# Optimization experiments

Hardware: AMD Instinct MI355X
Metric: run time of the kernel (lower is better)

## Reference

```python
import jax, jax.numpy as jnp
import numpy as np

NUM_CODES = 128
BETA = 0.25


def conv1d(x, w, b):
    # x: (B, C, T), w: (O, I, K) torch layout, 'same' padding for k=3
    y = jax.lax.conv_general_dilated(x, w, window_strides=(1,), padding=[(1, 1)],
                                     dimension_numbers=('NCH', 'OIH', 'NCH'))
    return y + b[None, :, None]


def setup_inputs() -> dict:
    key = jax.random.key(0)
    ks = jax.random.split(key, 8)
    B, C, T, K = 16, 192, 8192, NUM_CODES
    fan = 1.0 / np.sqrt(C * 3)
    inp = {
        'x': jax.random.normal(ks[0], (B, C, T), jnp.float32),
        'enc_w1': jax.random.normal(ks[1], (C, C, 3), jnp.float32) * fan,
        'enc_b1': jnp.zeros((C,), jnp.float32),
        'enc_w2': jax.random.normal(ks[2], (C, C, 3), jnp.float32) * fan,
        'enc_b2': jnp.zeros((C,), jnp.float32),
        'emb': jax.random.normal(ks[3], (K, C), jnp.float32) * (1.0 / K),
        'dec_w1': jax.random.normal(ks[4], (C, C, 3), jnp.float32) * fan,
        'dec_b1': jnp.zeros((C,), jnp.float32),
        'dec_w2': jax.random.normal(ks[5], (C, C, 3), jnp.float32) * fan,
        'dec_b2': jnp.zeros((C,), jnp.float32),
        'dec_w3': jax.random.normal(ks[6], (C, C, 3), jnp.float32) * fan,
        'dec_b3': jnp.zeros((C,), jnp.float32),
    }
    return inp


def vector_quantize(z_e, emb):
    # z_e: (B, C, T) -> tokens (B*T, C)
    B, C, T = z_e.shape
    z = jnp.transpose(z_e, (0, 2, 1)).reshape(-1, C)          # (N, C)
    # squared distances ||z||^2 + ||e||^2 - 2 z.e
    d = (jnp.sum(z * z, axis=1, keepdims=True)
         + jnp.sum(emb * emb, axis=1)[None, :]
         - 2.0 * (z @ emb.T))                                  # (N, K)
    idx = jnp.argmin(d, axis=1)                                # (N,)
    z_q = emb[idx]                                             # (N, C) gather
    # loss = ||sg(z_q) - z||^2*... standard: codebook + beta*commitment
    loss = (jnp.mean((jax.lax.stop_gradient(z_q) - z) ** 2)
            + BETA * jnp.mean((z_q - jax.lax.stop_gradient(z)) ** 2))
    # perplexity of code usage
    n = z.shape[0]
    counts = jnp.zeros((emb.shape[0],), z.dtype).at[idx].add(1.0)
    probs = counts / n
    perplexity = jnp.exp(-jnp.sum(probs * jnp.log(probs + 1e-10)))
    # straight-through
    z_q = z + jax.lax.stop_gradient(z_q - z)
    z_q = jnp.transpose(z_q.reshape(B, T, C), (0, 2, 1))
    return loss, z_q, perplexity, idx


def reference(x, enc_w1, enc_b1, enc_w2, enc_b2, emb,
              dec_w1, dec_b1, dec_w2, dec_b2, dec_w3, dec_b3):
    # encoder: conv -> relu -> conv
    z_e = conv1d(jax.nn.relu(conv1d(x, enc_w1, enc_b1)), enc_w2, enc_b2)
    embedding_loss, z_q, perplexity, _ = vector_quantize(z_e, emb)
    # NOTE: source forward decodes z_e (not z_q) — reproduced faithfully
    h = jax.nn.relu(conv1d(z_e, dec_w1, dec_b1))
    h = jax.nn.relu(conv1d(h, dec_w2, dec_b2))
    x_hat = conv1d(h, dec_w3, dec_b3)
    return embedding_loss, x_hat, perplexity
```

## Files before the change

### kernel.cpp

```cpp
#include <hip/hip_runtime.h>
#include <hip/hip_bf16.h>
#include <stdint.h>

typedef short s16x8 __attribute__((ext_vector_type(8)));
typedef float f32x4 __attribute__((ext_vector_type(4)));
typedef unsigned int u32;
typedef unsigned short u16;

#define CCH 192
#define APITCH 200
#define NCODES 128
#define HALO 9
#define RPB 8216
#define LEAD 12
#define TOK 128
#define AROWS 146
#define WSTRIDE 40960

__device__ __forceinline__ u16 f2b(float f) {
  u32 u = __builtin_bit_cast(u32, f);
  u = (u + 0x7fffu + ((u >> 16) & 1u)) >> 16;
  return (u16)u;
}
__device__ __forceinline__ float b2f(u16 h) {
  return __builtin_bit_cast(float, ((u32)h) << 16);
}
__device__ __forceinline__ void gld16(const void* g, void* l) {
  __builtin_amdgcn_global_load_lds(
      (const __attribute__((address_space(1))) void*)g,
      (__attribute__((address_space(3))) void*)l, 16, 0, 0);
}

__global__ __launch_bounds__(256) void k_tin(const float* __restrict__ x, u16* __restrict__ xtp,
                                             int B, int T) {
  __shared__ float tile[32][36];
  int nt = T >> 5;
  int bid = blockIdx.x;
  int b = bid / (6 * nt);
  int rem = bid % (6 * nt);
  int cb = rem / nt, tb = rem % nt;
  int tid = threadIdx.x;
  {
    int c = tid >> 3, seg = tid & 7;
    const float* src = x + ((size_t)b * CCH + cb * 32 + c) * T + tb * 32 + seg * 4;
    float4 v = *(const float4*)src;
    tile[c][seg * 4 + 0] = v.x; tile[c][seg * 4 + 1] = v.y;
    tile[c][seg * 4 + 2] = v.z; tile[c][seg * 4 + 3] = v.w;
  }
  __syncthreads();
  {
    int t = tid >> 3, cs = tid & 7;
    u16* dst = xtp + ((size_t)(b * RPB + LEAD + tb * 32 + t)) * APITCH + cb * 32 + cs * 4;
    ushort4 o;
    o.x = f2b(tile[cs * 4 + 0][t]); o.y = f2b(tile[cs * 4 + 1][t]);
    o.z = f2b(tile[cs * 4 + 2][t]); o.w = f2b(tile[cs * 4 + 3][t]);
    *(ushort4*)dst = o;
  }
}

__global__ __launch_bounds__(256) void k_padz(u16* __restrict__ xtp) {
  int b = blockIdx.x;
  for (int i = threadIdx.x; i < 24 * 25; i += 256) {
    int r = i / 25, c = i - (i / 25) * 25;
    int row = (r < 12) ? r : (RPB - 12 + (r - 12));
    uint4 z = {0u, 0u, 0u, 0u};
    *(uint4*)((char*)xtp + ((size_t)(b * RPB + row)) * 400 + c * 16) = z;
  }
}

__global__ __launch_bounds__(256) void k_wconv(const float* __restrict__ w, u16* __restrict__ dst) {
  int i = blockIdx.x * 256 + threadIdx.x;
  if (i >= 3 * CCH * CCH) return;
  int cb = i / 18432;
  int r = i - cb * 18432;
  int k = r / 6144;
  int r2 = r - k * 6144;
  int o = r2 / 32, il = r2 - o * 32;
  dst[cb * 20480 + k * 6144 + (il >> 3) * 1536 + o * 8 + (il & 7)] =
      f2b(w[(o * CCH + cb * 32 + il) * 3 + k]);
}

__global__ __launch_bounds__(64) void k_emb(const float* __restrict__ emb, u16* __restrict__ embp,
                                            float* __restrict__ e2) {
  int code = blockIdx.x, lane = threadIdx.x;
  float s = 0.f;
  for (int j = lane * 3; j < lane * 3 + 3; ++j) {
    float v = emb[code * CCH + j];
    embp[code * APITCH + j] = f2b(v);
    s += v * v;
  }
  if (lane < 8) embp[code * APITCH + 192 + lane] = 0;
  #pragma unroll
  for (int m = 1; m < 64; m <<= 1) s += __shfl_xor(s, m, 64);
  if (lane == 0) e2[code] = s;
}

__global__ void k_zero(int* hist, double* dsum) {
  int t = threadIdx.x;
  if (t < NCODES) hist[t] = 0;
  if (t == 0) *dsum = 0.0;
}

template<int G0, bool RELU, bool ISSUE_NEXT>
__device__ __forceinline__ void stage(const char* __restrict__ wtp, u16* __restrict__ act,
                                      u16 (*wb)[20480], const float* bv,
                                      int oB, const u16* arow, int rbase,
                                      int wv, int lane, int lr, int lg,
                                      int t0, int T, bool edge) {
  f32x4 acc[5][3];
  #pragma unroll
  for (int m = 0; m < 5; ++m)
    #pragma unroll
    for (int n = 0; n < 3; ++n) acc[m][n] = f32x4{0.f, 0.f, 0.f, 0.f};
  #pragma unroll
  for (int cb = 0; cb < 6; ++cb) {
    const int g = G0 + cb;
    asm volatile("s_waitcnt vmcnt(0)" ::: "memory");
    __builtin_amdgcn_sched_barrier(0);
    __builtin_amdgcn_s_barrier();
    if (cb < 5 || ISSUE_NEXT) {
      const char* src = wtp + (size_t)(g + 1) * WSTRIDE + (wv * 5) * 1024 + lane * 16;
      char* dst = (char*)wb[(g + 1) & 1] + (wv * 5) * 1024;
      #pragma unroll
      for (int j = 0; j < 5; ++j) gld16(src + j * 1024, dst + j * 1024);
    }
    const u16* wq = wb[g & 1] + lg * 1536;
    #pragma unroll
    for (int k = 0; k < 3; ++k) {
      s16x8 af[5];
      #pragma unroll
      for (int m = 0; m < 5; ++m)
        af[m] = *(const s16x8*)(arow + (16 * m + k) * APITCH + cb * 32);
      #pragma unroll
      for (int nf = 0; nf < 3; ++nf) {
        s16x8 wf = *(const s16x8*)(wq + k * 6144 + (oB + nf * 16 + lr) * 8);
        #pragma unroll
        for (int m = 0; m < 5; ++m)
          acc[m][nf] = __builtin_amdgcn_mfma_f32_16x16x32_bf16(af[m], wf, acc[m][nf], 0, 0, 0);
      }
    }
  }
  __builtin_amdgcn_s_barrier();
  if (!edge) {
    #pragma unroll
    for (int m = 0; m < 5; ++m)
      #pragma unroll
      for (int nf = 0; nf < 3; ++nf) {
        int o = oB + nf * 16 + lr;
        #pragma unroll
        for (int r = 0; r < 4; ++r) {
          int row = rbase + 16 * m + lg * 4 + r;
          float v = acc[m][nf][r] + bv[nf];
          if (RELU) v = fmaxf(v, 0.f);
          act[row * APITCH + o] = f2b(v);
        }
      }
  } else {
    #pragma unroll
    for (int m = 0; m < 5; ++m)
      #pragma unroll
      for (int nf = 0; nf < 3; ++nf) {
        int o = oB + nf * 16 + lr;
        #pragma unroll
        for (int r = 0; r < 4; ++r) {
          int row = rbase + 16 * m + lg * 4 + r;
          int tok = t0 - HALO + row;
          float v = acc[m][nf][r] + bv[nf];
          if (RELU) v = fmaxf(v, 0.f);
          if (tok < 0 || tok >= T) v = 0.f;
          act[row * APITCH + o] = f2b(v);
        }
      }
  }
  asm volatile("s_waitcnt lgkmcnt(0)" ::: "memory");
  __builtin_amdgcn_s_barrier();
}

__global__ __launch_bounds__(512, 1) void k_fused(
    const char* __restrict__ xtp, const char* __restrict__ wtp,
    const float* __restrict__ eb1, const float* __restrict__ eb2,
    const float* __restrict__ db1, const float* __restrict__ db2, const float* __restrict__ db3,
    const char* __restrict__ embp, const float* __restrict__ e2,
    int* __restrict__ hist, double* __restrict__ dsum,
    float* __restrict__ xhat, int T) {
  __shared__ __align__(16) u16 act[AROWS * APITCH];
  __shared__ __align__(16) u16 wb[2][20480];
  __shared__ int hs[NCODES];
  __shared__ float wsum[8];
  const int tid = threadIdx.x;
  const int wv = tid >> 6, lane = tid & 63, lr = lane & 15, lg = lane >> 4;
  const int nw = wv & 3, mw = wv >> 2;
  const int bid = blockIdx.x;
  const int b = bid >> 6, tile = bid & 63;
  const int t0 = tile * TOK;
  const bool edge = (tile == 0) || (tile == 63);
  const int oB = nw * 48;
  const int rbase = 1 + mw * 64;
  const u16* arow = act + (rbase - 1 + lr) * APITCH + lg * 8;
  if (tid < NCODES) hs[tid] = 0;

  float bvv[5][3];
  #pragma unroll
  for (int nf = 0; nf < 3; ++nf) {
    int o = oB + nf * 16 + lr;
    bvv[0][nf] = eb1[o]; bvv[1][nf] = eb2[o];
    bvv[2][nf] = db1[o]; bvv[3][nf] = db2[o]; bvv[4][nf] = db3[o];
  }

  {
    const char* src = xtp + (size_t)(b * RPB + LEAD + t0 - HALO) * 400;
    #pragma unroll
    for (int s = 0; s < 8; ++s) {
      int c = tid + s * 512;
      if (c < AROWS * 25)
        gld16(src + (size_t)c * 16, (char*)act + (size_t)c * 16);
    }
  }
  {
    const char* s0 = wtp + (size_t)(wv * 5) * 1024 + lane * 16;
    char* d0 = (char*)wb[0] + (wv * 5) * 1024;
    #pragma unroll
    for (int j = 0; j < 5; ++j) gld16(s0 + j * 1024, d0 + j * 1024);
  }

  stage<0,  true,  true >(wtp, act, wb, bvv[0], oB, arow, rbase, wv, lane, lr, lg, t0, T, edge);
  stage<6,  false, false>(wtp, act, wb, bvv[1], oB, arow, rbase, wv, lane, lr, lg, t0, T, edge);

  {
    #pragma unroll
    for (int j = 0; j < 4; ++j) {
      int c = wv + 8 * j;
      if (c < 25) {
        gld16(embp + c * 1024 + lane * 16, (char*)wb[0] + c * 1024);
        gld16(embp + 25600 + c * 1024 + lane * 16, (char*)wb[1] + c * 1024);
      }
    }
    asm volatile("s_waitcnt vmcnt(0)" ::: "memory");
    __builtin_amdgcn_sched_barrier(0);
    __builtin_amdgcn_s_barrier();

    const int row = HALO + wv * 16 + lr;
    f32x4 va[8];
    #pragma unroll
    for (int n = 0; n < 8; ++n) va[n] = f32x4{0.f, 0.f, 0.f, 0.f};
    #pragma unroll
    for (int cb = 0; cb < 6; ++cb) {
      s16x8 az = *(const s16x8*)(act + row * APITCH + cb * 32 + lg * 8);
      #pragma unroll
      for (int n = 0; n < 4; ++n) {
        s16x8 e1f = *(const s16x8*)(wb[0] + (n * 16 + lr) * APITCH + cb * 32 + lg * 8);
        va[n] = __builtin_amdgcn_mfma_f32_16x16x32_bf16(az, e1f, va[n], 0, 0, 0);
        s16x8 e2f = *(const s16x8*)(wb[1] + (n * 16 + lr) * APITCH + cb * 32 + lg * 8);
        va[n + 4] = __builtin_amdgcn_mfma_f32_16x16x32_bf16(az, e2f, va[n + 4], 0, 0, 0);
      }
    }
    float z2 = 0.f;
    const u16* zr = act + row * APITCH + lg * 48;
    #pragma unroll
    for (int j = 0; j < 48; j += 8) {
      s16x8 vv = *(const s16x8*)(zr + j);
      #pragma unroll
      for (int e = 0; e < 8; ++e) { float f = b2f((u16)vv[e]); z2 += f * f; }
    }
    z2 += __shfl_xor(z2, 16, 64);
    z2 += __shfl_xor(z2, 32, 64);
    float smin[4]; int imin[4];
    #pragma unroll
    for (int r = 0; r < 4; ++r) { smin[r] = 3.4e38f; imin[r] = 0; }
    #pragma unroll
    for (int n = 0; n < 8; ++n) {
      int code = n * 16 + lr;
      float ev = e2[code];
      #pragma unroll
      for (int r = 0; r < 4; ++r) {
        float sc = ev - 2.f * va[n][r];
        if (sc < smin[r]) { smin[r] = sc; imin[r] = code; }
      }
    }
    #pragma unroll
    for (int m = 1; m < 16; m <<= 1) {
      #pragma unroll
      for (int r = 0; r < 4; ++r) {
        float so = __shfl_xor(smin[r], m, 64);
        int io = __shfl_xor(imin[r], m, 64);
        if (so < smin[r] || (so == smin[r] && io < imin[r])) { smin[r] = so; imin[r] = io; }
      }
    }
    float z2t[4];
    #pragma unroll
    for (int r = 0; r < 4; ++r) z2t[r] = __shfl(z2, lg * 4 + r, 64);
    float dpart = 0.f;
    if (lr == 0) {
      #pragma unroll
      for (int r = 0; r < 4; ++r) {
        dpart += z2t[r] + smin[r];
        atomicAdd(&hs[imin[r]], 1);
      }
    }
    #pragma unroll
    for (int m = 1; m < 64; m <<= 1) dpart += __shfl_xor(dpart, m, 64);
    if (lane == 0) wsum[wv] = dpart;
    asm volatile("s_waitcnt lgkmcnt(0)" ::: "memory");
    __builtin_amdgcn_s_barrier();
    {
      const char* s = wtp + (size_t)12 * WSTRIDE + (wv * 5) * 1024 + lane * 16;
      char* d = (char*)wb[0] + (wv * 5) * 1024;
      #pragma unroll
      for (int j = 0; j < 5; ++j) gld16(s + j * 1024, d + j * 1024);
    }
    if (tid == 0) {
      double tot = 0.0;
      #pragma unroll
      for (int w = 0; w < 8; ++w) tot += (double)wsum[w];
      atomicAdd(dsum, tot);
    }
    if (tid < NCODES && hs[tid] > 0) atomicAdd(&hist[tid], hs[tid]);
  }

  stage<12, true, true>(wtp, act, wb, bvv[2], oB, arow, rbase, wv, lane, lr, lg, t0, T, edge);
  stage<18, true, true>(wtp, act, wb, bvv[3], oB, arow, rbase, wv, lane, lr, lg, t0, T, edge);

  f32x4 acc5[4][3];
  #pragma unroll
  for (int m = 0; m < 4; ++m)
    #pragma unroll
    for (int n = 0; n < 3; ++n) acc5[m][n] = f32x4{0.f, 0.f, 0.f, 0.f};
  {
    const u16* arow3 = act + (8 + mw * 64 + lr) * APITCH + lg * 8;
    #pragma unroll
    for (int cb = 0; cb < 6; ++cb) {
      const int g = 24 + cb;
      asm volatile("s_waitcnt vmcnt(0)" ::: "memory");
      __builtin_amdgcn_sched_barrier(0);
      __builtin_amdgcn_s_barrier();
      if (cb < 5) {
        const char* src = wtp + (size_t)(g + 1) * WSTRIDE + (wv * 5) * 1024 + lane * 16;
        char* dst = (char*)wb[(g + 1) & 1] + (wv * 5) * 1024;
        #pragma unroll
        for (int j = 0; j < 5; ++j) gld16(src + j * 1024, dst + j * 1024);
      }
      const u16* wq = wb[g & 1] + lg * 1536;
      #pragma unroll
      for (int k = 0; k < 3; ++k) {
        s16x8 af[4];
        #pragma unroll
        for (int m = 0; m < 4; ++m)
          af[m] = *(const s16x8*)(arow3 + (16 * m + k) * APITCH + cb * 32);
        #pragma unroll
        for (int nf = 0; nf < 3; ++nf) {
          s16x8 wf = *(const s16x8*)(wq + k * 6144 + (oB + nf * 16 + lr) * 8);
          #pragma unroll
          for (int m = 0; m < 4; ++m)
            acc5[m][nf] = __builtin_amdgcn_mfma_f32_16x16x32_bf16(af[m], wf, acc5[m][nf], 0, 0, 0);
        }
      }
    }
  }

  float* ft = (float*)act;
  float* dstb = xhat + (size_t)b * CCH * T + t0;
  #pragma unroll
  for (int p = 0; p < 2; ++p) {
    __builtin_amdgcn_s_barrier();
    if ((nw >> 1) == p) {
      #pragma unroll
      for (int m = 0; m < 4; ++m)
        #pragma unroll
        for (int nf = 0; nf < 3; ++nf) {
          int o = (nw & 1) * 48 + nf * 16 + lr;
          #pragma unroll
          for (int r = 0; r < 4; ++r) {
            int tl = mw * 64 + 16 * m + lg * 4 + r;
            ft[o * 130 + tl] = acc5[m][nf][r] + bvv[4][nf];
          }
        }
    }
    asm volatile("s_waitcnt lgkmcnt(0)" ::: "memory");
    __builtin_amdgcn_s_barrier();
    #pragma unroll
    for (int i = 0; i < 24; ++i) {
      int s = tid + i * 512;
      int o = s >> 7, tl = s & 127;
      dstb[(size_t)(o + p * 96) * T + tl] = ft[o * 130 + tl];
    }
  }
}

__global__ __launch_bounds__(128) void k_fin(const int* __restrict__ hist,
                                             const double* __restrict__ dsum,
                                             float* __restrict__ out, int N, int ppos) {
  __shared__ float H[NCODES];
  int t = threadIdx.x;
  float p = (float)hist[t] / (float)N;
  H[t] = p * logf(p + 1e-10f);
  __syncthreads();
  if (t == 0) {
    float s = 0.f;
    for (int i = 0; i < NCODES; ++i) s += H[i];
    out[ppos] = expf(-s);
    out[0] = (float)(1.25 * (*dsum) / ((double)N * (double)CCH));
  }
}

extern "C" void kernel_launch(void* const* d_in, const int* in_sizes, int n_in,
                              void* d_out, int out_size, void* d_ws, size_t ws_size,
                              hipStream_t stream) {
  const int B = 16, T = 8192, N = B * T;
  const float* x   = (const float*)d_in[0];
  const float* ew1 = (const float*)d_in[1];
  const float* eb1 = (const float*)d_in[2];
  const float* ew2 = (const float*)d_in[3];
  const float* eb2 = (const float*)d_in[4];
  const float* emb = (const float*)d_in[5];
  const float* dw1 = (const float*)d_in[6];
  const float* db1 = (const float*)d_in[7];
  const float* dw2 = (const float*)d_in[8];
  const float* db2 = (const float*)d_in[9];
  const float* dw3 = (const float*)d_in[10];
  const float* db3 = (const float*)d_in[11];

  char* ws = (char*)d_ws;
  char*  xtp  = ws;
  char*  wtp  = ws + 52582400;
  char*  embp = ws + 53811200;
  float* e2   = (float*)(ws + 53876736);
  int*   hist = (int*)(ws + 53877248);
  double* dsum = (double*)(ws + 53877760);

  const int wblocks = (3 * CCH * CCH + 255) / 256;
  k_wconv<<<wblocks, 256, 0, stream>>>(ew1, (u16*)wtp);
  k_wconv<<<wblocks, 256, 0, stream>>>(ew2, (u16*)wtp + 6 * 20480);
  k_wconv<<<wblocks, 256, 0, stream>>>(dw1, (u16*)wtp + 12 * 20480);
  k_wconv<<<wblocks, 256, 0, stream>>>(dw2, (u16*)wtp + 18 * 20480);
  k_wconv<<<wblocks, 256, 0, stream>>>(dw3, (u16*)wtp + 24 * 20480);
  k_emb<<<NCODES, 64, 0, stream>>>(emb, (u16*)embp, e2);
  k_zero<<<1, 256, 0, stream>>>(hist, dsum);
  k_padz<<<B, 256, 0, stream>>>((u16*)xtp);
  k_tin<<<B * 6 * (T / 32), 256, 0, stream>>>(x, (u16*)xtp, B, T);

  k_fused<<<B * (T / TOK), 512, 0, stream>>>(xtp, wtp, eb1, eb2, db1, db2, db3,
                                             embp, e2, hist, dsum, (float*)d_out + 1, T);
  k_fin<<<1, 128, 0, stream>>>(hist, dsum, (float*)d_out, N, out_size - 1);
}
```

Before: 280.3 us.

## Double token tile to 256 and stream conv weights in per-tap chunks

```diff
diff --git a/kernel.cpp b/kernel.cpp
--- a/kernel.cpp
+++ b/kernel.cpp
@@ -13,9 +13,9 @@
 #define HALO 9
 #define RPB 8216
 #define LEAD 12
-#define TOK 128
-#define AROWS 146
-#define WSTRIDE 40960
+#define TOK 256
+#define AROWS 274
+#define CHS 16384
 
 __device__ __forceinline__ u16 f2b(float f) {
   u32 u = __builtin_bit_cast(u32, f);
@@ -76,7 +76,7 @@
   int k = r / 6144;
   int r2 = r - k * 6144;
   int o = r2 / 32, il = r2 - o * 32;
-  dst[cb * 20480 + k * 6144 + (il >> 3) * 1536 + o * 8 + (il & 7)] =
+  dst[(size_t)(cb * 3 + k) * (CHS / 2) + (il >> 3) * 1536 + o * 8 + (il & 7)] =
       f2b(w[(o * CCH + cb * 32 + il) * 3 + k]);
 }
 
@@ -86,10 +86,10 @@
   float s = 0.f;
   for (int j = lane * 3; j < lane * 3 + 3; ++j) {
     float v = emb[code * CCH + j];
-    embp[code * APITCH + j] = f2b(v);
+    int cb = j >> 5, il = j & 31;
+    embp[(size_t)cb * 4096 + (il >> 3) * 1024 + code * 8 + (il & 7)] = f2b(v);
     s += v * v;
   }
-  if (lane < 8) embp[code * APITCH + 192 + lane] = 0;
   #pragma unroll
   for (int m = 1; m < 64; m <<= 1) s += __shfl_xor(s, m, 64);
   if (lane == 0) e2[code] = s;
@@ -101,49 +101,54 @@
   if (t == 0) *dsum = 0.0;
 }
 
-template<int G0, bool RELU, bool ISSUE_NEXT>
-__device__ __forceinline__ void stage(const char* __restrict__ wtp, u16* __restrict__ act,
-                                      u16 (*wb)[20480], const float* bv,
-                                      int oB, const u16* arow, int rbase,
-                                      int wv, int lane, int lr, int lg,
-                                      int t0, int T, bool edge) {
-  f32x4 acc[5][3];
-  #pragma unroll
-  for (int m = 0; m < 5; ++m)
-    #pragma unroll
-    for (int n = 0; n < 3; ++n) acc[m][n] = f32x4{0.f, 0.f, 0.f, 0.f};
-  #pragma unroll
-  for (int cb = 0; cb < 6; ++cb) {
-    const int g = G0 + cb;
+__device__ __forceinline__ void issueW(const char* src, u16* dstb, int wv, int lane) {
+  const char* s0 = src + wv * 2048 + lane * 16;
+  char* d0 = (char*)dstb + wv * 2048 + lane * 16;
+  gld16(s0, d0);
+  gld16(s0 + 1024, d0 + 1024);
+}
+__device__ __forceinline__ void issueE(const char* src, u16* dstb, int tid) {
+  gld16(src + tid * 16, (char*)dstb + tid * 16);
+}
+
+template<int G0, int F, int NEXT>
+__device__ __forceinline__ void conv_phase(const char* __restrict__ wtp, const char* __restrict__ embp,
+                                           const u16* __restrict__ arow, u16 (*wb)[8192],
+                                           int oB, int lr, int lg, int wv, int lane, int tid,
+                                           f32x4 (&acc)[F][3]) {
+  #pragma unroll 2
+  for (int s = 0; s < 18; ++s) {
     asm volatile("s_waitcnt vmcnt(0)" ::: "memory");
     __builtin_amdgcn_sched_barrier(0);
     __builtin_amdgcn_s_barrier();
-    if (cb < 5 || ISSUE_NEXT) {
-      const char* src = wtp + (size_t)(g + 1) * WSTRIDE + (wv * 5) * 1024 + lane * 16;
-      char* dst = (char*)wb[(g + 1) & 1] + (wv * 5) * 1024;
-      #pragma unroll
-      for (int j = 0; j < 5; ++j) gld16(src + j * 1024, dst + j * 1024);
-    }
-    const u16* wq = wb[g & 1] + lg * 1536;
-    #pragma unroll
-    for (int k = 0; k < 3; ++k) {
-      s16x8 af[5];
-      #pragma unroll
-      for (int m = 0; m < 5; ++m)
-        af[m] = *(const s16x8*)(arow + (16 * m + k) * APITCH + cb * 32);
-      #pragma unroll
-      for (int nf = 0; nf < 3; ++nf) {
-        s16x8 wf = *(const s16x8*)(wq + k * 6144 + (oB + nf * 16 + lr) * 8);
-        #pragma unroll
-        for (int m = 0; m < 5; ++m)
-          acc[m][nf] = __builtin_amdgcn_mfma_f32_16x16x32_bf16(af[m], wf, acc[m][nf], 0, 0, 0);
-      }
-    }
-  }
+    if (s < 17) issueW(wtp + (size_t)(G0 + s + 1) * CHS, wb[(s + 1) & 1], wv, lane);
+    else if (NEXT == 1) issueW(wtp + (size_t)(G0 + 18) * CHS, wb[0], wv, lane);
+    else if (NEXT == 2) issueE(embp, wb[0], tid);
+    const int cb = s / 3, k = s - 3 * (s / 3);
+    const u16* wq = wb[s & 1] + lg * 1536 + (oB + lr) * 8;
+    const u16* ab = arow + k * APITCH + cb * 32;
+    s16x8 af[F];
+    #pragma unroll
+    for (int m = 0; m < F; ++m)
+      af[m] = *(const s16x8*)(ab + 16 * m * APITCH);
+    #pragma unroll
+    for (int nf = 0; nf < 3; ++nf) {
+      s16x8 wf = *(const s16x8*)(wq + nf * 128);
+      #pragma unroll
+      for (int m = 0; m < F; ++m)
+        acc[m][nf] = __builtin_amdgcn_mfma_f32_16x16x32_bf16(af[m], wf, acc[m][nf], 0, 0, 0);
+    }
+  }
+}
+
+template<int F, bool RELU>
+__device__ __forceinline__ void writeback(u16* __restrict__ act, const f32x4 (&acc)[F][3],
+                                          const float* bv, int oB, int lr, int lg, int rbase,
+                                          int t0, int T, bool edge) {
   __builtin_amdgcn_s_barrier();
   if (!edge) {
     #pragma unroll
-    for (int m = 0; m < 5; ++m)
+    for (int m = 0; m < F; ++m)
       #pragma unroll
       for (int nf = 0; nf < 3; ++nf) {
         int o = oB + nf * 16 + lr;
@@ -157,7 +162,7 @@
       }
   } else {
     #pragma unroll
-    for (int m = 0; m < 5; ++m)
+    for (int m = 0; m < F; ++m)
       #pragma unroll
       for (int nf = 0; nf < 3; ++nf) {
         int o = oB + nf * 16 + lr;
@@ -176,7 +181,7 @@
   __builtin_amdgcn_s_barrier();
 }
 
-__global__ __launch_bounds__(512, 1) void k_fused(
+__global__ __launch_bounds__(512, 2) void k_fused(
     const char* __restrict__ xtp, const char* __restrict__ wtp,
     const float* __restrict__ eb1, const float* __restrict__ eb2,
     const float* __restrict__ db1, const float* __restrict__ db2, const float* __restrict__ db3,
@@ -184,18 +189,18 @@
     int* __restrict__ hist, double* __restrict__ dsum,
     float* __restrict__ xhat, int T) {
   __shared__ __align__(16) u16 act[AROWS * APITCH];
-  __shared__ __align__(16) u16 wb[2][20480];
+  __shared__ __align__(16) u16 wb[2][8192];
   __shared__ int hs[NCODES];
   __shared__ float wsum[8];
   const int tid = threadIdx.x;
   const int wv = tid >> 6, lane = tid & 63, lr = lane & 15, lg = lane >> 4;
   const int nw = wv & 3, mw = wv >> 2;
   const int bid = blockIdx.x;
-  const int b = bid >> 6, tile = bid & 63;
+  const int b = bid >> 5, tile = bid & 31;
   const int t0 = tile * TOK;
-  const bool edge = (tile == 0) || (tile == 63);
+  const bool edge = (tile == 0) || (tile == 31);
   const int oB = nw * 48;
-  const int rbase = 1 + mw * 64;
+  const int rbase = 1 + mw * 128;
   const u16* arow = act + (rbase - 1 + lr) * APITCH + lg * 8;
   if (tid < NCODES) hs[tid] = 0;
 
@@ -210,91 +215,99 @@
   {
     const char* src = xtp + (size_t)(b * RPB + LEAD + t0 - HALO) * 400;
     #pragma unroll
-    for (int s = 0; s < 8; ++s) {
+    for (int s = 0; s < 14; ++s) {
       int c = tid + s * 512;
       if (c < AROWS * 25)
         gld16(src + (size_t)c * 16, (char*)act + (size_t)c * 16);
     }
   }
-  {
-    const char* s0 = wtp + (size_t)(wv * 5) * 1024 + lane * 16;
-    char* d0 = (char*)wb[0] + (wv * 5) * 1024;
-    #pragma unroll
-    for (int j = 0; j < 5; ++j) gld16(s0 + j * 1024, d0 + j * 1024);
-  }
-
-  stage<0,  true,  true >(wtp, act, wb, bvv[0], oB, arow, rbase, wv, lane, lr, lg, t0, T, edge);
-  stage<6,  false, false>(wtp, act, wb, bvv[1], oB, arow, rbase, wv, lane, lr, lg, t0, T, edge);
-
-  {
-    #pragma unroll
-    for (int j = 0; j < 4; ++j) {
-      int c = wv + 8 * j;
-      if (c < 25) {
-        gld16(embp + c * 1024 + lane * 16, (char*)wb[0] + c * 1024);
-        gld16(embp + 25600 + c * 1024 + lane * 16, (char*)wb[1] + c * 1024);
-      }
-    }
-    asm volatile("s_waitcnt vmcnt(0)" ::: "memory");
-    __builtin_amdgcn_sched_barrier(0);
-    __builtin_amdgcn_s_barrier();
-
-    const int row = HALO + wv * 16 + lr;
-    f32x4 va[8];
-    #pragma unroll
-    for (int n = 0; n < 8; ++n) va[n] = f32x4{0.f, 0.f, 0.f, 0.f};
-    #pragma unroll
-    for (int cb = 0; cb < 6; ++cb) {
-      s16x8 az = *(const s16x8*)(act + row * APITCH + cb * 32 + lg * 8);
-      #pragma unroll
-      for (int n = 0; n < 4; ++n) {
-        s16x8 e1f = *(const s16x8*)(wb[0] + (n * 16 + lr) * APITCH + cb * 32 + lg * 8);
-        va[n] = __builtin_amdgcn_mfma_f32_16x16x32_bf16(az, e1f, va[n], 0, 0, 0);
-        s16x8 e2f = *(const s16x8*)(wb[1] + (n * 16 + lr) * APITCH + cb * 32 + lg * 8);
-        va[n + 4] = __builtin_amdgcn_mfma_f32_16x16x32_bf16(az, e2f, va[n + 4], 0, 0, 0);
-      }
-    }
-    float z2 = 0.f;
-    const u16* zr = act + row * APITCH + lg * 48;
-    #pragma unroll
-    for (int j = 0; j < 48; j += 8) {
-      s16x8 vv = *(const s16x8*)(zr + j);
-      #pragma unroll
-      for (int e = 0; e < 8; ++e) { float f = b2f((u16)vv[e]); z2 += f * f; }
-    }
-    z2 += __shfl_xor(z2, 16, 64);
-    z2 += __shfl_xor(z2, 32, 64);
-    float smin[4]; int imin[4];
-    #pragma unroll
-    for (int r = 0; r < 4; ++r) { smin[r] = 3.4e38f; imin[r] = 0; }
-    #pragma unroll
-    for (int n = 0; n < 8; ++n) {
-      int code = n * 16 + lr;
-      float ev = e2[code];
+  issueW(wtp, wb[0], wv, lane);
+
+  {
+    f32x4 acc[9][3];
+    #pragma unroll
+    for (int m = 0; m < 9; ++m)
+      #pragma unroll
+      for (int n = 0; n < 3; ++n) acc[m][n] = f32x4{0.f, 0.f, 0.f, 0.f};
+    conv_phase<0, 9, 1>(wtp, embp, arow, wb, oB, lr, lg, wv, lane, tid, acc);
+    writeback<9, true>(act, acc, bvv[0], oB, lr, lg, rbase, t0, T, edge);
+  }
+  {
+    f32x4 acc[9][3];
+    #pragma unroll
+    for (int m = 0; m < 9; ++m)
+      #pragma unroll
+      for (int n = 0; n < 3; ++n) acc[m][n] = f32x4{0.f, 0.f, 0.f, 0.f};
+    conv_phase<18, 9, 2>(wtp, embp, arow, wb, oB, lr, lg, wv, lane, tid, acc);
+    writeback<9, false>(act, acc, bvv[1], oB, lr, lg, rbase, t0, T, edge);
+  }
+
+  {
+    f32x4 va0[8], va1[8];
+    #pragma unroll
+    for (int n = 0; n < 8; ++n) { va0[n] = f32x4{0.f,0.f,0.f,0.f}; va1[n] = f32x4{0.f,0.f,0.f,0.f}; }
+    const int zr0 = 9 + wv * 32 + lr;
+    #pragma unroll 2
+    for (int s = 0; s < 6; ++s) {
+      asm volatile("s_waitcnt vmcnt(0)" ::: "memory");
+      __builtin_amdgcn_sched_barrier(0);
+      __builtin_amdgcn_s_barrier();
+      if (s < 5) issueE(embp + (s + 1) * 8192, wb[(s + 1) & 1], tid);
+      else issueW(wtp + (size_t)36 * CHS, wb[0], wv, lane);
+      const u16* eq = wb[s & 1] + lg * 1024 + lr * 8;
+      s16x8 az0 = *(const s16x8*)(act + zr0 * APITCH + s * 32 + lg * 8);
+      s16x8 az1 = *(const s16x8*)(act + (zr0 + 16) * APITCH + s * 32 + lg * 8);
+      #pragma unroll
+      for (int nf = 0; nf < 8; ++nf) {
+        s16x8 ef = *(const s16x8*)(eq + nf * 128);
+        va0[nf] = __builtin_amdgcn_mfma_f32_16x16x32_bf16(az0, ef, va0[nf], 0, 0, 0);
+        va1[nf] = __builtin_amdgcn_mfma_f32_16x16x32_bf16(az1, ef, va1[nf], 0, 0, 0);
+      }
+    }
+    float e2v[8];
+    #pragma unroll
+    for (int nf = 0; nf < 8; ++nf) e2v[nf] = e2[nf * 16 + lr];
+    float dpart = 0.f;
+    #pragma unroll
+    for (int rg = 0; rg < 2; ++rg) {
+      float z2 = 0.f;
+      const u16* zr = act + (zr0 + rg * 16) * APITCH + lg * 48;
+      #pragma unroll
+      for (int j = 0; j < 48; j += 8) {
+        s16x8 vv = *(const s16x8*)(zr + j);
+        #pragma unroll
+        for (int e = 0; e < 8; ++e) { float f = b2f((u16)vv[e]); z2 += f * f; }
+      }
+      z2 += __shfl_xor(z2, 16, 64);
+      z2 += __shfl_xor(z2, 32, 64);
+      float smin[4]; int imin[4];
+      #pragma unroll
+      for (int r = 0; r < 4; ++r) { smin[r] = 3.4e38f; imin[r] = 0; }
+      #pragma unroll
+      for (int nf = 0; nf < 8; ++nf) {
+        int code = nf * 16 + lr;
+        #pragma unroll
+        for (int r = 0; r < 4; ++r) {
+          float sc = e2v[nf] - 2.f * (rg ? va1[nf][r] : va0[nf][r]);
+          if (sc < smin[r]) { smin[r] = sc; imin[r] = code; }
+        }
+      }
+      #pragma unroll
+      for (int m = 1; m < 16; m <<= 1) {
+        #pragma unroll
+        for (int r = 0; r < 4; ++r) {
+          float so = __shfl_xor(smin[r], m, 64);
+          int io = __shfl_xor(imin[r], m, 64);
+          if (so < smin[r] || (so == smin[r] && io < imin[r])) { smin[r] = so; imin[r] = io; }
+        }
+      }
       #pragma unroll
       for (int r = 0; r < 4; ++r) {
-        float sc = ev - 2.f * va[n][r];
-        if (sc < smin[r]) { smin[r] = sc; imin[r] = code; }
-      }
-    }
-    #pragma unroll
-    for (int m = 1; m < 16; m <<= 1) {
-      #pragma unroll
-      for (int r = 0; r < 4; ++r) {
-        float so = __shfl_xor(smin[r], m, 64);
-        int io = __shfl_xor(imin[r], m, 64);
-        if (so < smin[r] || (so == smin[r] && io < imin[r])) { smin[r] = so; imin[r] = io; }
-      }
-    }
-    float z2t[4];
-    #pragma unroll
-    for (int r = 0; r < 4; ++r) z2t[r] = __shfl(z2, lg * 4 + r, 64);
-    float dpart = 0.f;
-    if (lr == 0) {
-      #pragma unroll
-      for (int r = 0; r < 4; ++r) {
-        dpart += z2t[r] + smin[r];
-        atomicAdd(&hs[imin[r]], 1);
+        float z2t = __shfl(z2, lg * 4 + r, 64);
+        if (lr == 0) {
+          dpart += z2t + smin[r];
+          atomicAdd(&hs[imin[r]], 1);
+        }
       }
     }
     #pragma unroll
@@ -302,12 +315,6 @@
     if (lane == 0) wsum[wv] = dpart;
     asm volatile("s_waitcnt lgkmcnt(0)" ::: "memory");
     __builtin_amdgcn_s_barrier();
-    {
-      const char* s = wtp + (size_t)12 * WSTRIDE + (wv * 5) * 1024 + lane * 16;
-      char* d = (char*)wb[0] + (wv * 5) * 1024;
-      #pragma unroll
-      for (int j = 0; j < 5; ++j) gld16(s + j * 1024, d + j * 1024);
-    }
     if (tid == 0) {
       double tot = 0.0;
       #pragma unroll
@@ -317,44 +324,33 @@
     if (tid < NCODES && hs[tid] > 0) atomicAdd(&hist[tid], hs[tid]);
   }
 
-  stage<12, true, true>(wtp, act, wb, bvv[2], oB, arow, rbase, wv, lane, lr, lg, t0, T, edge);
-  stage<18, true, true>(wtp, act, wb, bvv[3], oB, arow, rbase, wv, lane, lr, lg, t0, T, edge);
-
-  f32x4 acc5[4][3];
+  {
+    f32x4 acc[9][3];
+    #pragma unroll
+    for (int m = 0; m < 9; ++m)
+      #pragma unroll
+      for (int n = 0; n < 3; ++n) acc[m][n] = f32x4{0.f, 0.f, 0.f, 0.f};
+    conv_phase<36, 9, 1>(wtp, embp, arow, wb, oB, lr, lg, wv, lane, tid, acc);
+    writeback<9, true>(act, acc, bvv[2], oB, lr, lg, rbase, t0, T, edge);
+  }
+  {
+    f32x4 acc[9][3];
+    #pragma unroll
+    for (int m = 0; m < 9; ++m)
+      #pragma unroll
+      for (int n = 0; n < 3; ++n) acc[m][n] = f32x4{0.f, 0.f, 0.f, 0.f};
+    conv_phase<54, 9, 1>(wtp, embp, arow, wb, oB, lr, lg, wv, lane, tid, acc);
+    writeback<9, true>(act, acc, bvv[3], oB, lr, lg, rbase, t0, T, edge);
+  }
+
+  f32x4 acc5[8][3];
   #pragma unroll
-  for (int m = 0; m < 4; ++m)
+  for (int m = 0; m < 8; ++m)
     #pragma unroll
     for (int n = 0; n < 3; ++n) acc5[m][n] = f32x4{0.f, 0.f, 0.f, 0.f};
   {
-    const u16* arow3 = act + (8 + mw * 64 + lr) * APITCH + lg * 8;
-    #pragma unroll
-    for (int cb = 0; cb < 6; ++cb) {
-      const int g = 24 + cb;
-      asm volatile("s_waitcnt vmcnt(0)" ::: "memory");
-      __builtin_amdgcn_sched_barrier(0);
-      __builtin_amdgcn_s_barrier();
-      if (cb < 5) {
-        const char* src = wtp + (size_t)(g + 1) * WSTRIDE + (wv * 5) * 1024 + lane * 16;
-        char* dst = (char*)wb[(g + 1) & 1] + (wv * 5) * 1024;
-        #pragma unroll
-        for (int j = 0; j < 5; ++j) gld16(src + j * 1024, dst + j * 1024);
-      }
-      const u16* wq = wb[g & 1] + lg * 1536;
-      #pragma unroll
-      for (int k = 0; k < 3; ++k) {
-        s16x8 af[4];
-        #pragma unroll
-        for (int m = 0; m < 4; ++m)
-          af[m] = *(const s16x8*)(arow3 + (16 * m + k) * APITCH + cb * 32);
-        #pragma unroll
-        for (int nf = 0; nf < 3; ++nf) {
-          s16x8 wf = *(const s16x8*)(wq + k * 6144 + (oB + nf * 16 + lr) * 8);
-          #pragma unroll
-          for (int m = 0; m < 4; ++m)
-            acc5[m][nf] = __builtin_amdgcn_mfma_f32_16x16x32_bf16(af[m], wf, acc5[m][nf], 0, 0, 0);
-        }
-      }
-    }
+    const u16* arow3 = act + (8 + mw * 128 + lr) * APITCH + lg * 8;
+    conv_phase<72, 8, 0>(wtp, embp, arow3, wb, oB, lr, lg, wv, lane, tid, acc5);
   }
 
   float* ft = (float*)act;
@@ -364,24 +360,24 @@
     __builtin_amdgcn_s_barrier();
     if ((nw >> 1) == p) {
       #pragma unroll
-      for (int m = 0; m < 4; ++m)
+      for (int m = 0; m < 8; ++m)
         #pragma unroll
         for (int nf = 0; nf < 3; ++nf) {
           int o = (nw & 1) * 48 + nf * 16 + lr;
           #pragma unroll
           for (int r = 0; r < 4; ++r) {
-            int tl = mw * 64 + 16 * m + lg * 4 + r;
-            ft[o * 130 + tl] = acc5[m][nf][r] + bvv[4][nf];
+            int tl = mw * 128 + 16 * m + lg * 4 + r;
+            ft[o * 260 + tl] = acc5[m][nf][r] + bvv[4][nf];
           }
         }
     }
     asm volatile("s_waitcnt lgkmcnt(0)" ::: "memory");
     __builtin_amdgcn_s_barrier();
     #pragma unroll
-    for (int i = 0; i < 24; ++i) {
+    for (int i = 0; i < 48; ++i) {
       int s = tid + i * 512;
-      int o = s >> 7, tl = s & 127;
-      dstb[(size_t)(o + p * 96) * T + tl] = ft[o * 130 + tl];
+      int o = s >> 8, tl = s & 255;
+      dstb[(size_t)(o + p * 96) * T + tl] = ft[o * 260 + tl];
     }
   }
 }
@@ -421,18 +417,19 @@
 
   char* ws = (char*)d_ws;
   char*  xtp  = ws;
-  char*  wtp  = ws + 52582400;
-  char*  embp = ws + 53811200;
-  float* e2   = (float*)(ws + 53876736);
-  int*   hist = (int*)(ws + 53877248);
-  double* dsum = (double*)(ws + 53877760);
+  char*  wtp  = ws + 52583424;
+  char*  embp = ws + 54057984;
+  float* e2   = (float*)(ws + 54107136);
+  int*   hist = (int*)(ws + 54107648);
+  double* dsum = (double*)(ws + 54108160);
 
   const int wblocks = (3 * CCH * CCH + 255) / 256;
+  const int TCH = 18 * (CHS / 2);
   k_wconv<<<wblocks, 256, 0, stream>>>(ew1, (u16*)wtp);
-  k_wconv<<<wblocks, 256, 0, stream>>>(ew2, (u16*)wtp + 6 * 20480);
-  k_wconv<<<wblocks, 256, 0, stream>>>(dw1, (u16*)wtp + 12 * 20480);
-  k_wconv<<<wblocks, 256, 0, stream>>>(dw2, (u16*)wtp + 18 * 20480);
-  k_wconv<<<wblocks, 256, 0, stream>>>(dw3, (u16*)wtp + 24 * 20480);
+  k_wconv<<<wblocks, 256, 0, stream>>>(ew2, (u16*)wtp + TCH);
+  k_wconv<<<wblocks, 256, 0, stream>>>(dw1, (u16*)wtp + 2 * TCH);
+  k_wconv<<<wblocks, 256, 0, stream>>>(dw2, (u16*)wtp + 3 * TCH);
+  k_wconv<<<wblocks, 256, 0, stream>>>(dw3, (u16*)wtp + 4 * TCH);
   k_emb<<<NCODES, 64, 0, stream>>>(emb, (u16*)embp, e2);
   k_zero<<<1, 256, 0, stream>>>(hist, dsum);
   k_padz<<<B, 256, 0, stream>>>((u16*)xtp);
```

After: 273.6 us. 1.02x faster.
